# Performance work log

Measured on AMD Instinct MI355X. Metric: run time of the kernel, lower is better.

Reference implementation:

```python
import jax, jax.numpy as jnp
import numpy as np

D_MODEL = 1024
NUM_HEADS = 16
HEAD_DIM = D_MODEL // NUM_HEADS
SCALE = float(np.sqrt(HEAD_DIM))


def _xavier(key, shape):
    fan_out, fan_in = shape
    lim = float(np.sqrt(6.0 / (fan_in + fan_out)))
    return jax.random.uniform(key, shape, jnp.float32, -lim, lim)


def setup_inputs() -> dict:
    key = jax.random.key(0)
    kx, kqkv, ko = jax.random.split(key, 3)
    B, T = 2, 2048
    x = jax.random.normal(kx, (B, T, D_MODEL), jnp.float32)
    W_qkv = _xavier(kqkv, (3 * D_MODEL, D_MODEL))  # torch Linear weight [out, in]
    b_qkv = jnp.zeros((3 * D_MODEL,), jnp.float32)
    W_o = _xavier(ko, (D_MODEL, D_MODEL))
    b_o = jnp.zeros((D_MODEL,), jnp.float32)
    return {"x": x, "W_qkv": W_qkv, "b_qkv": b_qkv, "W_o": W_o, "b_o": b_o}


def reference(x, W_qkv, b_qkv, W_o, b_o):
    B, T, C = x.shape
    qkv = x @ W_qkv.T + b_qkv                       # [B, T, 3C]
    qkv = qkv.reshape(B, T, 3, NUM_HEADS, HEAD_DIM)
    qkv = jnp.transpose(qkv, (2, 0, 3, 1, 4))       # [3, B, H, T, d]
    Q, K, V = qkv[0], qkv[1], qkv[2]
    scores = jnp.einsum("bhqd,bhkd->bhqk", Q, K) / SCALE
    attn = jax.nn.softmax(scores, axis=-1)          # dropout p=0 -> identity
    out = jnp.einsum("bhqk,bhkd->bhqd", attn, V)    # [B, H, T, d]
    out = jnp.transpose(out, (0, 2, 1, 3)).reshape(B, T, C)
    return out @ W_o.T + b_o
```

## Files before the change

kernel.cpp:

```cpp
#include <hip/hip_runtime.h>
#include <math.h>

#define B_ 2
#define T_ 2048
#define C_ 1024
#define H_ 16
#define M_ (B_*T_)
#define QKVSZ (B_*H_*T_*64)

typedef _Float16 f16;
typedef _Float16 f16x8 __attribute__((ext_vector_type(8)));
typedef float f32x4 __attribute__((ext_vector_type(4)));

#define GLL16(g, l) __builtin_amdgcn_global_load_lds(                     \
    (const __attribute__((address_space(1))) void*)(g),                   \
    (__attribute__((address_space(3))) void*)(l), 16, 0, 0)

#define DRAIN_SYNC() do {                                                 \
    asm volatile("s_waitcnt vmcnt(0) lgkmcnt(0)" ::: "memory");           \
    __builtin_amdgcn_sched_barrier(0);                                    \
    __syncthreads();                                                      \
} while (0)

__global__ __launch_bounds__(256) void cvt_kernel(const float* __restrict__ x,
                                                  const float* __restrict__ wq,
                                                  const float* __restrict__ wo,
                                                  f16* __restrict__ xf,
                                                  f16* __restrict__ wqf,
                                                  f16* __restrict__ wof) {
    const int b = blockIdx.x;
    const float* src;
    f16* dst;
    size_t off;
    if (b < 2048)      { src = x;  dst = xf;  off = (size_t)b * 2048; }
    else if (b < 3584) { src = wq; dst = wqf; off = (size_t)(b - 2048) * 2048; }
    else               { src = wo; dst = wof; off = (size_t)(b - 3584) * 2048; }
    const size_t e = off + (size_t)threadIdx.x * 8;
    const float4 v0 = *(const float4*)(src + e);
    const float4 v1 = *(const float4*)(src + e + 4);
    f16x8 r = {(f16)v0.x, (f16)v0.y, (f16)v0.z, (f16)v0.w,
               (f16)v1.x, (f16)v1.y, (f16)v1.z, (f16)v1.w};
    *(f16x8*)(dst + e) = r;
}

template <int WRITE_MODE>
__global__ __launch_bounds__(256) void gemm_f16(const f16* __restrict__ Af,
                                                const f16* __restrict__ Bf,
                                                const float* __restrict__ bias,
                                                void* __restrict__ out,
                                                int nbm) {
    __shared__ __align__(16) f16 At[2][128 * 32];
    __shared__ __align__(16) f16 Bt[2][128 * 32];

    const int tid = threadIdx.x;
    const int l = tid & 63;
    const int w = tid >> 6;
    const int c = l & 15, g = l >> 4;
    const int wr = w >> 1, wc = w & 1;
    const int bm = blockIdx.x % nbm, bn = blockIdx.x / nbm;

    const f16* Ag = Af + (size_t)(bm * 128 + w * 32 + (l >> 2)) * 1024 + (l & 3) * 8;
    const f16* Bg = Bf + (size_t)(bn * 128 + w * 32 + (l >> 2)) * 1024 + (l & 3) * 8;

    f32x4 acc[4][4];
#pragma unroll
    for (int mt = 0; mt < 4; ++mt)
#pragma unroll
        for (int nt = 0; nt < 4; ++nt) {
            f32x4 z = {0.f, 0.f, 0.f, 0.f};
            acc[mt][nt] = z;
        }

    GLL16(Ag,         &At[0][w * 1024]);
    GLL16(Ag + 16384, &At[0][w * 1024 + 512]);
    GLL16(Bg,         &Bt[0][w * 1024]);
    GLL16(Bg + 16384, &Bt[0][w * 1024 + 512]);
    DRAIN_SYNC();

    int cur = 0;
    for (int ks = 0; ks < 32; ++ks) {
        if (ks < 31) {
            const int k0 = (ks + 1) * 32;
            GLL16(Ag + k0,         &At[cur ^ 1][w * 1024]);
            GLL16(Ag + k0 + 16384, &At[cur ^ 1][w * 1024 + 512]);
            GLL16(Bg + k0,         &Bt[cur ^ 1][w * 1024]);
            GLL16(Bg + k0 + 16384, &Bt[cur ^ 1][w * 1024 + 512]);
        }
        const f16* Acur = At[cur];
        const f16* Bcur = Bt[cur];
        f16x8 af[4];
#pragma unroll
        for (int mt = 0; mt < 4; ++mt)
            af[mt] = *(const f16x8*)(Acur + (wr * 64 + mt * 16 + c) * 32 + g * 8);
#pragma unroll
        for (int nt = 0; nt < 4; ++nt) {
            const f16x8 bfr = *(const f16x8*)(Bcur + (wc * 64 + nt * 16 + c) * 32 + g * 8);
#pragma unroll
            for (int mt = 0; mt < 4; ++mt)
                acc[mt][nt] = __builtin_amdgcn_mfma_f32_16x16x32_f16(af[mt], bfr, acc[mt][nt], 0, 0, 0);
        }
        DRAIN_SYNC();
        cur ^= 1;
    }

#pragma unroll
    for (int mt = 0; mt < 4; ++mt)
#pragma unroll
        for (int nt = 0; nt < 4; ++nt)
#pragma unroll
            for (int r = 0; r < 4; ++r) {
                const int m = bm * 128 + wr * 64 + mt * 16 + g * 4 + r;
                const int n = bn * 128 + wc * 64 + nt * 16 + c;
                const float val = acc[mt][nt][r] + bias[n];
                if (WRITE_MODE == 0) {
                    const int s = n >> 10, h = (n >> 6) & 15, d = n & 63;
                    const int b = m >> 11, t = m & 2047;
                    const int bh = b * H_ + h;
                    f16* base = (f16*)out;
                    if (s == 0) {
                        base[((size_t)(bh * T_ + t)) * 64 + d] = (f16)(val * 0.125f);
                    } else {
                        const int tile = t >> 6, row = t & 63;
                        if (s == 1) {
                            const int ch = (d >> 3) ^ (row & 7);
                            base[(size_t)QKVSZ +
                                 ((size_t)((bh * 32 + tile) * 64 + row)) * 64 + ch * 8 + (d & 7)] = (f16)val;
                        } else {
                            const int cj = (row >> 3) ^ (d & 7);
                            base[(size_t)(2 * QKVSZ) +
                                 ((size_t)((bh * 32 + tile) * 64 + d)) * 64 + cj * 8 + (row & 7)] = (f16)val;
                        }
                    }
                } else {
                    ((float*)out)[(size_t)m * C_ + n] = val;
                }
            }
}

__global__ __launch_bounds__(256) void attn_mfma(const f16* __restrict__ Qf,
                                                 const f16* __restrict__ Kf,
                                                 const f16* __restrict__ Vf,
                                                 f16* __restrict__ AO) {
    __shared__ __align__(16) f16 Kh[64 * 64];
    __shared__ __align__(16) f16 Vt[64 * 64];
    __shared__ __align__(16) f16 Pl[4][16 * 64];

    const int tid = threadIdx.x;
    const int lane = tid & 63;
    const int w = tid >> 6;
    const int g = lane >> 4;
    const int c = lane & 15;

    const int bh = blockIdx.x & 31;
    const int qt = blockIdx.x >> 5;

    const f16* Qp = Qf + ((size_t)(bh * T_ + qt * 64 + w * 16 + c)) * 64 + g * 8;
    const f16x8 qa0 = *(const f16x8*)(Qp);
    const f16x8 qa1 = *(const f16x8*)(Qp + 32);

    f32x4 o[4];
    float mrow[4], lsum[4];
#pragma unroll
    for (int i = 0; i < 4; ++i) {
        f32x4 z = {0.f, 0.f, 0.f, 0.f};
        o[i] = z;
        mrow[i] = -INFINITY;
        lsum[i] = 0.f;
    }

    const f16* Ktile = Kf + (size_t)bh * 32 * 4096;
    const f16* Vtile = Vf + (size_t)bh * 32 * 4096;

    const int soff0 = (w * 128 + lane) * 8;
    const int soff1 = (w * 128 + 64 + lane) * 8;

    uint4 kr0 = *(const uint4*)(Ktile + soff0);
    uint4 kr1 = *(const uint4*)(Ktile + soff1);
    uint4 vr0 = *(const uint4*)(Vtile + soff0);
    uint4 vr1 = *(const uint4*)(Vtile + soff1);

    f16* const Pw = Pl[w];

    for (int kt = 0; kt < 32; ++kt) {
        DRAIN_SYNC();
        *(uint4*)(Kh + soff0) = kr0;
        *(uint4*)(Kh + soff1) = kr1;
        *(uint4*)(Vt + soff0) = vr0;
        *(uint4*)(Vt + soff1) = vr1;
        DRAIN_SYNC();

        if (kt < 31) {
            const f16* Kn = Ktile + (size_t)(kt + 1) * 4096;
            const f16* Vn = Vtile + (size_t)(kt + 1) * 4096;
            kr0 = *(const uint4*)(Kn + soff0);
            kr1 = *(const uint4*)(Kn + soff1);
            vr0 = *(const uint4*)(Vn + soff0);
            vr1 = *(const uint4*)(Vn + soff1);
        }

        f32x4 s[4];
#pragma unroll
        for (int jt = 0; jt < 4; ++jt) {
            f32x4 z = {0.f, 0.f, 0.f, 0.f};
            s[jt] = z;
        }
#pragma unroll
        for (int ks = 0; ks < 2; ++ks) {
            const f16x8 qa = ks ? qa1 : qa0;
#pragma unroll
            for (int jt = 0; jt < 4; ++jt) {
                const int row = jt * 16 + c;
                const f16x8 kb = *(const f16x8*)(Kh + row * 64 + (((ks * 4 + g) ^ (row & 7)) * 8));
                s[jt] = __builtin_amdgcn_mfma_f32_16x16x32_f16(qa, kb, s[jt], 0, 0, 0);
            }
        }

        float al[4];
#pragma unroll
        for (int r = 0; r < 4; ++r) {
            float mx = fmaxf(fmaxf(s[0][r], s[1][r]), fmaxf(s[2][r], s[3][r]));
            mx = fmaxf(mx, __shfl_xor(mx, 1));
            mx = fmaxf(mx, __shfl_xor(mx, 2));
            mx = fmaxf(mx, __shfl_xor(mx, 4));
            mx = fmaxf(mx, __shfl_xor(mx, 8));
            const float mn = fmaxf(mrow[r], mx);
            al[r] = __expf(mrow[r] - mn);
            mrow[r] = mn;
            float ps = 0.f;
#pragma unroll
            for (int jt = 0; jt < 4; ++jt) {
                const float p = __expf(s[jt][r] - mn);
                s[jt][r] = p;
                ps += p;
            }
            lsum[r] = lsum[r] * al[r] + ps;
        }

#pragma unroll
        for (int jt = 0; jt < 4; ++jt)
#pragma unroll
            for (int r = 0; r < 4; ++r) {
                const int row = g * 4 + r;
                const int ch = (jt * 2 + (c >> 3)) ^ (row & 7);
                Pw[row * 64 + ch * 8 + (c & 7)] = (f16)s[jt][r];
            }
        asm volatile("s_waitcnt lgkmcnt(0)" ::: "memory");
        __builtin_amdgcn_sched_barrier(0);

#pragma unroll
        for (int dt = 0; dt < 4; ++dt)
#pragma unroll
            for (int r = 0; r < 4; ++r) o[dt][r] *= al[r];

#pragma unroll
        for (int ks = 0; ks < 2; ++ks) {
            const f16x8 pa = *(const f16x8*)(Pw + c * 64 + (((ks * 4 + g) ^ (c & 7)) * 8));
#pragma unroll
            for (int dt = 0; dt < 4; ++dt) {
                const int row = dt * 16 + c;
                const f16x8 vb = *(const f16x8*)(Vt + row * 64 + (((ks * 4 + g) ^ (row & 7)) * 8));
                o[dt] = __builtin_amdgcn_mfma_f32_16x16x32_f16(pa, vb, o[dt], 0, 0, 0);
            }
        }
    }

#pragma unroll
    for (int r = 0; r < 4; ++r) {
        float v = lsum[r];
        v += __shfl_xor(v, 1);
        v += __shfl_xor(v, 2);
        v += __shfl_xor(v, 4);
        v += __shfl_xor(v, 8);
        lsum[r] = 1.f / v;
    }
    const int b = bh >> 4, h = bh & 15;
#pragma unroll
    for (int dt = 0; dt < 4; ++dt)
#pragma unroll
        for (int r = 0; r < 4; ++r) {
            const int row = qt * 64 + w * 16 + g * 4 + r;
            AO[((size_t)(b * T_ + row)) * C_ + h * 64 + dt * 16 + c] = (f16)(o[dt][r] * lsum[r]);
        }
}

extern "C" void kernel_launch(void* const* d_in, const int* in_sizes, int n_in,
                              void* d_out, int out_size, void* d_ws, size_t ws_size,
                              hipStream_t stream) {
    const float* x     = (const float*)d_in[0];
    const float* W_qkv = (const float*)d_in[1];
    const float* b_qkv = (const float*)d_in[2];
    const float* W_o   = (const float*)d_in[3];
    const float* b_o   = (const float*)d_in[4];

    f16* ws16 = (f16*)d_ws;
    f16* xf  = ws16;
    f16* wqf = xf + 4194304;
    f16* wof = wqf + 3145728;
    f16* Qf  = wof + 1048576;
    f16* AOf = Qf + (size_t)3 * QKVSZ;

    cvt_kernel<<<dim3(4096), dim3(256), 0, stream>>>(x, W_qkv, W_o, xf, wqf, wof);

    gemm_f16<0><<<dim3(32 * 24), dim3(256), 0, stream>>>(xf, wqf, b_qkv, (void*)Qf, 32);

    attn_mfma<<<dim3(32 * 32), dim3(256), 0, stream>>>(Qf, Qf + QKVSZ, Qf + 2 * QKVSZ, AOf);

    gemm_f16<1><<<dim3(32 * 8), dim3(256), 0, stream>>>(AOf, wof, b_o, d_out, 32);
}
```

Before: 241.1 us.

## Double-buffer K/V in LDS and transpose QK^T MFMA to cut softmax shuffles

The attention kernel now keeps two LDS buffers for K and V. The next tile is stored to LDS while the current one is being computed, with global loads issued two tiles ahead, which replaces the two full drains and barriers per iteration with a single LDS-count barrier. The QK^T MFMA operands are swapped so each lane holds one query row's scores. The row max and sum then need only two cross-lane shuffles, and P is written as packed 4-wide stores, at the cost of per-row alpha and inverse broadcasts via __shfl. It doubles K/V LDS usage and adds register pressure, which may affect occupancy.

```diff
diff --git a/kernel.cpp b/kernel.cpp
--- a/kernel.cpp
+++ b/kernel.cpp
@@ -9,6 +9,7 @@
 #define QKVSZ (B_*H_*T_*64)
 
 typedef _Float16 f16;
+typedef _Float16 f16x4 __attribute__((ext_vector_type(4)));
 typedef _Float16 f16x8 __attribute__((ext_vector_type(8)));
 typedef float f32x4 __attribute__((ext_vector_type(4)));
 
@@ -20,6 +21,13 @@
     asm volatile("s_waitcnt vmcnt(0) lgkmcnt(0)" ::: "memory");           \
     __builtin_amdgcn_sched_barrier(0);                                    \
     __syncthreads();                                                      \
+} while (0)
+
+#define LGKM_BAR() do {                                                   \
+    asm volatile("s_waitcnt lgkmcnt(0)" ::: "memory");                    \
+    __builtin_amdgcn_sched_barrier(0);                                    \
+    __builtin_amdgcn_s_barrier();                                         \
+    __builtin_amdgcn_sched_barrier(0);                                    \
 } while (0)
 
 __global__ __launch_bounds__(256) void cvt_kernel(const float* __restrict__ x,
@@ -141,8 +149,8 @@
                                                  const f16* __restrict__ Kf,
                                                  const f16* __restrict__ Vf,
                                                  f16* __restrict__ AO) {
-    __shared__ __align__(16) f16 Kh[64 * 64];
-    __shared__ __align__(16) f16 Vt[64 * 64];
+    __shared__ __align__(16) f16 Kh[2][64 * 64];
+    __shared__ __align__(16) f16 Vt[2][64 * 64];
     __shared__ __align__(16) f16 Pl[4][16 * 64];
 
     const int tid = threadIdx.x;
@@ -159,14 +167,12 @@
     const f16x8 qa1 = *(const f16x8*)(Qp + 32);
 
     f32x4 o[4];
-    float mrow[4], lsum[4];
 #pragma unroll
     for (int i = 0; i < 4; ++i) {
         f32x4 z = {0.f, 0.f, 0.f, 0.f};
         o[i] = z;
-        mrow[i] = -INFINITY;
-        lsum[i] = 0.f;
     }
+    float mrow = -INFINITY, lsum = 0.f;
 
     const f16* Ktile = Kf + (size_t)bh * 32 * 4096;
     const f16* Vtile = Vf + (size_t)bh * 32 * 4096;
@@ -174,29 +180,28 @@
     const int soff0 = (w * 128 + lane) * 8;
     const int soff1 = (w * 128 + 64 + lane) * 8;
 
-    uint4 kr0 = *(const uint4*)(Ktile + soff0);
-    uint4 kr1 = *(const uint4*)(Ktile + soff1);
-    uint4 vr0 = *(const uint4*)(Vtile + soff0);
-    uint4 vr1 = *(const uint4*)(Vtile + soff1);
+    {
+        uint4 a = *(const uint4*)(Ktile + soff0);
+        uint4 b = *(const uint4*)(Ktile + soff1);
+        uint4 cc = *(const uint4*)(Vtile + soff0);
+        uint4 d = *(const uint4*)(Vtile + soff1);
+        *(uint4*)(&Kh[0][soff0]) = a;
+        *(uint4*)(&Kh[0][soff1]) = b;
+        *(uint4*)(&Vt[0][soff0]) = cc;
+        *(uint4*)(&Vt[0][soff1]) = d;
+    }
+    uint4 kr0 = *(const uint4*)(Ktile + 4096 + soff0);
+    uint4 kr1 = *(const uint4*)(Ktile + 4096 + soff1);
+    uint4 vr0 = *(const uint4*)(Vtile + 4096 + soff0);
+    uint4 vr1 = *(const uint4*)(Vtile + 4096 + soff1);
+    LGKM_BAR();
 
     f16* const Pw = Pl[w];
 
     for (int kt = 0; kt < 32; ++kt) {
-        DRAIN_SYNC();
-        *(uint4*)(Kh + soff0) = kr0;
-        *(uint4*)(Kh + soff1) = kr1;
-        *(uint4*)(Vt + soff0) = vr0;
-        *(uint4*)(Vt + soff1) = vr1;
-        DRAIN_SYNC();
-
-        if (kt < 31) {
-            const f16* Kn = Ktile + (size_t)(kt + 1) * 4096;
-            const f16* Vn = Vtile + (size_t)(kt + 1) * 4096;
-            kr0 = *(const uint4*)(Kn + soff0);
-            kr1 = *(const uint4*)(Kn + soff1);
-            vr0 = *(const uint4*)(Vn + soff0);
-            vr1 = *(const uint4*)(Vn + soff1);
-        }
+        const int cb = kt & 1;
+        const f16* Kc = Kh[cb];
+        const f16* Vc = Vt[cb];
 
         f32x4 s[4];
 #pragma unroll
@@ -210,47 +215,64 @@
 #pragma unroll
             for (int jt = 0; jt < 4; ++jt) {
                 const int row = jt * 16 + c;
-                const f16x8 kb = *(const f16x8*)(Kh + row * 64 + (((ks * 4 + g) ^ (row & 7)) * 8));
-                s[jt] = __builtin_amdgcn_mfma_f32_16x16x32_f16(qa, kb, s[jt], 0, 0, 0);
+                const f16x8 kb = *(const f16x8*)(Kc + row * 64 + (((ks * 4 + g) ^ (row & 7)) * 8));
+                s[jt] = __builtin_amdgcn_mfma_f32_16x16x32_f16(kb, qa, s[jt], 0, 0, 0);
             }
         }
 
-        float al[4];
-#pragma unroll
-        for (int r = 0; r < 4; ++r) {
-            float mx = fmaxf(fmaxf(s[0][r], s[1][r]), fmaxf(s[2][r], s[3][r]));
-            mx = fmaxf(mx, __shfl_xor(mx, 1));
-            mx = fmaxf(mx, __shfl_xor(mx, 2));
-            mx = fmaxf(mx, __shfl_xor(mx, 4));
-            mx = fmaxf(mx, __shfl_xor(mx, 8));
-            const float mn = fmaxf(mrow[r], mx);
-            al[r] = __expf(mrow[r] - mn);
-            mrow[r] = mn;
-            float ps = 0.f;
-#pragma unroll
-            for (int jt = 0; jt < 4; ++jt) {
+        if (kt < 31) {
+            f16* Kn = Kh[cb ^ 1];
+            f16* Vn = Vt[cb ^ 1];
+            *(uint4*)(Kn + soff0) = kr0;
+            *(uint4*)(Kn + soff1) = kr1;
+            *(uint4*)(Vn + soff0) = vr0;
+            *(uint4*)(Vn + soff1) = vr1;
+        }
+        if (kt < 30) {
+            const f16* Kg2 = Ktile + (size_t)(kt + 2) * 4096;
+            const f16* Vg2 = Vtile + (size_t)(kt + 2) * 4096;
+            kr0 = *(const uint4*)(Kg2 + soff0);
+            kr1 = *(const uint4*)(Kg2 + soff1);
+            vr0 = *(const uint4*)(Vg2 + soff0);
+            vr1 = *(const uint4*)(Vg2 + soff1);
+        }
+
+        float mx = s[0][0];
+#pragma unroll
+        for (int jt = 0; jt < 4; ++jt)
+#pragma unroll
+            for (int r = 0; r < 4; ++r) mx = fmaxf(mx, s[jt][r]);
+        mx = fmaxf(mx, __shfl_xor(mx, 16));
+        mx = fmaxf(mx, __shfl_xor(mx, 32));
+        const float mn = fmaxf(mrow, mx);
+        const float alpha = __expf(mrow - mn);
+        mrow = mn;
+        float ps = 0.f;
+#pragma unroll
+        for (int jt = 0; jt < 4; ++jt)
+#pragma unroll
+            for (int r = 0; r < 4; ++r) {
                 const float p = __expf(s[jt][r] - mn);
                 s[jt][r] = p;
                 ps += p;
             }
-            lsum[r] = lsum[r] * al[r] + ps;
-        }
-
-#pragma unroll
-        for (int jt = 0; jt < 4; ++jt)
-#pragma unroll
-            for (int r = 0; r < 4; ++r) {
-                const int row = g * 4 + r;
-                const int ch = (jt * 2 + (c >> 3)) ^ (row & 7);
-                Pw[row * 64 + ch * 8 + (c & 7)] = (f16)s[jt][r];
-            }
+        lsum = lsum * alpha + ps;
+
+#pragma unroll
+        for (int jt = 0; jt < 4; ++jt) {
+            f16x4 v = {(f16)s[jt][0], (f16)s[jt][1], (f16)s[jt][2], (f16)s[jt][3]};
+            *(f16x4*)(Pw + c * 64 + (((2 * jt + (g >> 1)) ^ (c & 7)) * 8) + 4 * (g & 1)) = v;
+        }
         asm volatile("s_waitcnt lgkmcnt(0)" ::: "memory");
         __builtin_amdgcn_sched_barrier(0);
 
+        float alr[4];
+#pragma unroll
+        for (int r = 0; r < 4; ++r) alr[r] = __shfl(alpha, g * 4 + r);
 #pragma unroll
         for (int dt = 0; dt < 4; ++dt)
 #pragma unroll
-            for (int r = 0; r < 4; ++r) o[dt][r] *= al[r];
+            for (int r = 0; r < 4; ++r) o[dt][r] *= alr[r];
 
 #pragma unroll
         for (int ks = 0; ks < 2; ++ks) {
@@ -258,28 +280,29 @@
 #pragma unroll
             for (int dt = 0; dt < 4; ++dt) {
                 const int row = dt * 16 + c;
-                const f16x8 vb = *(const f16x8*)(Vt + row * 64 + (((ks * 4 + g) ^ (row & 7)) * 8));
+                const f16x8 vb = *(const f16x8*)(Vc + row * 64 + (((ks * 4 + g) ^ (row & 7)) * 8));
                 o[dt] = __builtin_amdgcn_mfma_f32_16x16x32_f16(pa, vb, o[dt], 0, 0, 0);
             }
         }
+
+        LGKM_BAR();
     }
 
-#pragma unroll
-    for (int r = 0; r < 4; ++r) {
-        float v = lsum[r];
-        v += __shfl_xor(v, 1);
-        v += __shfl_xor(v, 2);
-        v += __shfl_xor(v, 4);
-        v += __shfl_xor(v, 8);
-        lsum[r] = 1.f / v;
-    }
+    float L = lsum;
+    L += __shfl_xor(L, 16);
+    L += __shfl_xor(L, 32);
+    const float inv = 1.f / L;
+    float invr[4];
+#pragma unroll
+    for (int r = 0; r < 4; ++r) invr[r] = __shfl(inv, g * 4 + r);
+
     const int b = bh >> 4, h = bh & 15;
 #pragma unroll
     for (int dt = 0; dt < 4; ++dt)
 #pragma unroll
         for (int r = 0; r < 4; ++r) {
             const int row = qt * 64 + w * 16 + g * 4 + r;
-            AO[((size_t)(b * T_ + row)) * C_ + h * 64 + dt * 16 + c] = (f16)(o[dt][r] * lsum[r]);
+            AO[((size_t)(b * T_ + row)) * C_ + h * 64 + dt * 16 + c] = (f16)(o[dt][r] * invr[r]);
         }
 }
 
```

Measured after the change: 218.6 us. 9.4% less time.
